# Performance work log

Hardware: AMD Instinct MI355X
Metric: run time of the kernel (lower is better)

Reference implementation:

```python
import jax, jax.numpy as jnp
import numpy as np
import math


def _strided_value_mask(L, S, dtype):
    # mask_line[L + d] == 0 when |d| is a power-of-two stride in {2,4,...,<=L};
    # value_mask[i, j] = mask_line[L - i + j], i.e. zero where |j - i| is such a stride.
    diff = jnp.abs(jnp.arange(L)[:, None] - jnp.arange(S)[None, :])  # [L, S]
    vm = jnp.ones((L, S), dtype=dtype)
    stride = 2
    while stride <= L:
        vm = vm * (diff != stride).astype(dtype)
        stride *= 2
    return vm


def setup_inputs() -> dict:
    key = jax.random.key(0)
    k1, k2, k3 = jax.random.split(key, 3)
    B, L, H, E = 4, 2048, 8, 64
    D = 64
    return {
        "queries": jax.random.normal(k1, (B, L, H, E), dtype=jnp.float32),
        "keys": jax.random.normal(k2, (B, L, H, E), dtype=jnp.float32),
        "values": jax.random.normal(k3, (B, L, H, D), dtype=jnp.float32),
    }


def reference(queries, keys, values):
    B, L, H, E = queries.shape
    S = keys.shape[1]
    scale = 1.0 / math.sqrt(E)

    # raw scores [B, H, L, S]
    scores = jnp.einsum("blhe,bshe->bhls", queries, keys)
    # multiplicative strided mask (zeroes scores at power-of-two offsets)
    vm = _strided_value_mask(L, S, scores.dtype)  # [L, S]
    scores = scores * vm
    # causal mask: upper triangle -> -inf (mask_flag=True, attn_mask=None path)
    causal = jnp.triu(jnp.ones((L, S), dtype=bool), k=1)
    scores = jnp.where(causal, -jnp.inf, scores)

    # dropout p=0.0 (eval) -> identity
    A = jax.nn.softmax(scale * scores, axis=-1)
    V = jnp.einsum("bhls,bshd->blhd", A, values)
    return V
```

## Files before the change

### kernel.cpp

```cpp
#include <hip/hip_runtime.h>
#include <hip/hip_bf16.h>
#include <stdint.h>

typedef __attribute__((ext_vector_type(8))) short short8;
typedef __attribute__((ext_vector_type(16))) float f32x16;

namespace {
constexpr int NB = 4, NL = 2048, NH = 8, NE = 64, ND = 64;
constexpr int KVBLK = 32;
constexpr float KS = 0.125f * 1.44269504f;
constexpr int NCHUNK = 40;
constexpr int RECSZ = 8320;
}

__device__ const unsigned char TG[NCHUNK] = {
  3,7,7,11,11,11,15,15,15,15, 10,10,14,14,14,14, 6,6,9,10, 13,13,13,13,
  9,9, 12,12,12,12, 2,5,5, 8,8,8, 4,4, 1, 0};
__device__ const unsigned char TT0[NCHUNK] = {
  0,0,16,0,16,32,0,16,32,48, 0,15,0,15,30,45, 0,14,0,30, 0,14,28,42,
  14,27, 0,13,26,39, 0,0,12, 0,12,24, 0,10, 0, 0};
__device__ const unsigned char TT1[NCHUNK] = {
  16,16,32,16,32,48,16,32,48,64, 15,30,15,30,45,60, 14,28,14,44, 14,28,42,56,
  27,40, 13,26,39,52, 12,12,24, 12,24,36, 10,20, 8, 4};
__device__ const unsigned char TREC[NCHUNK] = {
  3,10,11,21,22,23,36,37,38,39, 18,19,32,33,34,35, 8,9,15,20, 28,29,30,31,
  16,17, 24,25,26,27, 2,6,7, 12,13,14, 4,5, 1, 0};
__device__ const unsigned char CUMD[16] = {0,1,2,3,4,6,8,10,12,15,18,21,24,28,32,36};
__device__ const unsigned char NCHD[16] = {1,1,1,1,2,2,2,2,3,3,3,3,4,4,4,4};

__device__ __forceinline__ ushort bfb(float x) {
  __hip_bfloat16 b(x);
  return __builtin_bit_cast(ushort, b);
}
__device__ __forceinline__ uint32_t pkbf(float lo, float hi) {
  return (uint32_t)bfb(lo) | ((uint32_t)bfb(hi) << 16);
}

__global__ __launch_bounds__(256, 4)
void sattn_part(const float* __restrict__ Qg, const float* __restrict__ Kg,
                const float* __restrict__ Vg, float* __restrict__ W)
{
  const int id = blockIdx.x;
  const int bh = id & 31;
  const int e  = id >> 5;
  const int g  = TG[e];
  const int t0 = TT0[e], t1 = TT1[e];
  float* rec = W + (size_t)(bh * NCHUNK + TREC[e]) * RECSZ;
  const int b = bh >> 3, h = bh & 7;

  const int tid  = threadIdx.x;
  const int wave = tid >> 6;
  const int lane = tid & 63;
  const int ln31 = lane & 31;
  const int hi   = lane >> 5;

  __shared__ __align__(16) struct {
    ushort kt[KVBLK * 64];
    ushort vt[64 * 40];
  } lds;

  const int q0w = g * 128 + wave * 32;
  const int qi  = q0w + ln31;
  const int tw  = 4 * g + wave;

  short8 qf[4];
  {
    const float* qp = Qg + (((size_t)b * NL + qi) * NH + h) * NE;
    #pragma unroll
    for (int st = 0; st < 4; ++st) {
      const float* qpe = qp + st * 16 + hi * 8;
      union { short8 v; uint32_t u[4]; } f;
      #pragma unroll
      for (int j = 0; j < 4; ++j)
        f.u[j] = pkbf(qpe[2 * j] * KS, qpe[2 * j + 1] * KS);
      qf[st] = f.v;
    }
  }

  f32x16 acc0, acc1;
  #pragma unroll
  for (int i = 0; i < 16; ++i) { acc0[i] = 0.f; acc1[i] = 0.f; }
  float ls = 0.f;

  const int krow = tid >> 3,        kcol = (tid & 7) * 8;
  const int vrow = (tid >> 4) * 2,  vcol = (tid & 15) * 4;
  const float* kpp = Kg + (((size_t)b * NL + t0 * KVBLK + krow) * NH + h) * NE + kcol;
  const float* vpp = Vg + (((size_t)b * NL + t0 * KVBLK + vrow) * NH + h) * ND + vcol;
  constexpr int KSTEP = KVBLK * NH * NE;

  float kx[8], vx[8];
  #pragma unroll
  for (int j = 0; j < 8; ++j) kx[j] = kpp[j];
  #pragma unroll
  for (int j = 0; j < 4; ++j) { vx[j] = vpp[j]; vx[4 + j] = vpp[j + NH * ND]; }

  for (int t = t0; t < t1; ++t) {
    const int kv0 = t * KVBLK;
    __syncthreads();
    {
      uint32_t* kd = (uint32_t*)((char*)lds.kt + krow * 128 +
                                 ((kcol * 2) ^ ((krow & 7) << 4)));
      kd[0] = pkbf(kx[0], kx[1]); kd[1] = pkbf(kx[2], kx[3]);
      kd[2] = pkbf(kx[4], kx[5]); kd[3] = pkbf(kx[6], kx[7]);
      #pragma unroll
      for (int j = 0; j < 4; ++j) {
        int d = vcol + j;
        *(uint32_t*)((char*)lds.vt + d * 80 +
                     ((vrow * 2) ^ (((d >> 3) & 3) << 4))) = pkbf(vx[j], vx[4 + j]);
      }
    }
    {
      int tn = (t + 1 < t1) ? t + 1 : t;
      const float* kp = kpp + (size_t)(tn - t0) * KSTEP;
      const float* vp = vpp + (size_t)(tn - t0) * KSTEP;
      #pragma unroll
      for (int j = 0; j < 8; ++j) kx[j] = kp[j];
      #pragma unroll
      for (int j = 0; j < 4; ++j) { vx[j] = vp[j]; vx[4 + j] = vp[j + NH * ND]; }
    }
    __syncthreads();
    if (t > tw) continue;

    f32x16 s;
    #pragma unroll
    for (int i = 0; i < 16; ++i) s[i] = 0.f;
    const char* kb  = (const char*)lds.kt + ln31 * 128;
    const int   ksw = (ln31 & 7) << 4;
    __builtin_amdgcn_s_setprio(1);
    #pragma unroll
    for (int st = 0; st < 4; ++st) {
      short8 kf = *(const short8*)(kb + ((st * 32 + hi * 16) ^ ksw));
      s = __builtin_amdgcn_mfma_f32_32x32x16_bf16(kf, qf[st], s, 0, 0, 0);
    }
    __builtin_amdgcn_s_setprio(0);

    const int delta = q0w - kv0;
    const int qrelh = (qi - kv0) - 4 * hi;
    float ps0 = 0, ps1 = 0;
    if (t == tw) {
      #pragma unroll
      for (int r = 0; r < 16; ++r) {
        const int cr = (r & 3) + 8 * (r >> 2);
        int diff = qrelh - cr;
        float lg = s[r];
        bool p2 = (diff > 1) & ((diff & (diff - 1)) == 0);
        lg = p2 ? 0.f : lg;
        lg = (diff < 0) ? -__builtin_inff() : lg;
        float p = exp2f(lg);
        s[r] = p; (r & 1 ? ps1 : ps0) += p;
      }
    } else {
      int pmax = 1 << (31 - __clz(delta + 31));
      if (pmax >= delta - 31) {
        #pragma unroll
        for (int r = 0; r < 16; ++r) {
          const int cr = (r & 3) + 8 * (r >> 2);
          int diff = qrelh - cr;
          bool p2 = (diff > 1) & ((diff & (diff - 1)) == 0);
          float p = exp2f(p2 ? 0.f : s[r]);
          s[r] = p; (r & 1 ? ps1 : ps0) += p;
        }
      } else {
        #pragma unroll
        for (int r = 0; r < 16; ++r) {
          float p = exp2f(s[r]);
          s[r] = p; (r & 1 ? ps1 : ps0) += p;
        }
      }
    }
    ls += ps0 + ps1;

    uint32_t w0 = pkbf(s[0],  s[1]),  w1 = pkbf(s[2],  s[3]);
    uint32_t w2 = pkbf(s[4],  s[5]),  w3 = pkbf(s[6],  s[7]);
    uint32_t w4 = pkbf(s[8],  s[9]),  w5 = pkbf(s[10], s[11]);
    uint32_t w6 = pkbf(s[12], s[13]), w7 = pkbf(s[14], s[15]);
    uint32_t y0 = __shfl_xor(hi ? w0 : w2, 32);
    uint32_t y1 = __shfl_xor(hi ? w1 : w3, 32);
    uint32_t y2 = __shfl_xor(hi ? w4 : w6, 32);
    uint32_t y3 = __shfl_xor(hi ? w5 : w7, 32);
    union { short8 v; uint32_t u[4]; } f0, f1;
    if (hi == 0) {
      f0.u[0] = w0; f0.u[1] = w1; f0.u[2] = y0; f0.u[3] = y1;
      f1.u[0] = w4; f1.u[1] = w5; f1.u[2] = y2; f1.u[3] = y3;
    } else {
      f0.u[0] = y0; f0.u[1] = y1; f0.u[2] = w2; f0.u[3] = w3;
      f1.u[0] = y2; f1.u[1] = y3; f1.u[2] = w6; f1.u[3] = w7;
    }

    const char* vb = (const char*)lds.vt;
    const int d0 = ln31,      sw0 = ((d0 >> 3) & 3) << 4;
    const int d1 = 32 + ln31, sw1 = ((d1 >> 3) & 3) << 4;
    short8 a00 = *(const short8*)(vb + d0 * 80 + ((hi * 16) ^ sw0));
    short8 a01 = *(const short8*)(vb + d0 * 80 + ((32 + hi * 16) ^ sw0));
    short8 a10 = *(const short8*)(vb + d1 * 80 + ((hi * 16) ^ sw1));
    short8 a11 = *(const short8*)(vb + d1 * 80 + ((32 + hi * 16) ^ sw1));
    __builtin_amdgcn_s_setprio(1);
    acc0 = __builtin_amdgcn_mfma_f32_32x32x16_bf16(a00, f0.v, acc0, 0, 0, 0);
    acc0 = __builtin_amdgcn_mfma_f32_32x32x16_bf16(a01, f1.v, acc0, 0, 0, 0);
    acc1 = __builtin_amdgcn_mfma_f32_32x32x16_bf16(a10, f0.v, acc1, 0, 0, 0);
    acc1 = __builtin_amdgcn_mfma_f32_32x32x16_bf16(a11, f1.v, acc1, 0, 0, 0);
    __builtin_amdgcn_s_setprio(0);
  }

  ls += __shfl_xor(ls, 32);
  #pragma unroll
  for (int r = 0; r < 16; ++r) {
    int d = (r & 3) + 8 * (r >> 2) + 4 * hi;
    rec[d * 128 + wave * 32 + ln31]        = acc0[r];
    rec[(32 + d) * 128 + wave * 32 + ln31] = acc1[r];
  }
  if (hi == 0) rec[8192 + wave * 32 + ln31] = ls;
}

__global__ __launch_bounds__(256)
void sattn_combine(const float* __restrict__ W, float* __restrict__ Og)
{
  const int id = blockIdx.x;
  const int h2 = id & 1, g = (id >> 1) & 15, bh = id >> 5;
  const int b = bh >> 3, h = bh & 7;
  const int tid = threadIdx.x;

  __shared__ float sd[64][66];
  __shared__ float Lq[64];

  const float* rec0 = W + (size_t)(bh * NCHUNK + CUMD[g]) * RECSZ;
  const int nc = NCHD[g];

  #pragma unroll
  for (int rep = 0; rep < 16; ++rep) {
    int lin = rep * 256 + tid;
    int q = lin & 63, d = lin >> 6;
    float a = 0.f;
    for (int c = 0; c < nc; ++c) a += rec0[c * RECSZ + d * 128 + h2 * 64 + q];
    sd[d][q] = a;
  }
  if (tid < 64) {
    float a = 0.f;
    for (int c = 0; c < nc; ++c) a += rec0[c * RECSZ + 8192 + h2 * 64 + tid];
    Lq[tid] = 1.0f / a;
  }
  __syncthreads();
  #pragma unroll
  for (int rep = 0; rep < 16; ++rep) {
    int d = tid & 63, q = rep * 4 + (tid >> 6);
    float v = sd[d][q] * Lq[q];
    Og[(((size_t)b * NL + g * 128 + h2 * 64 + q) * NH + h) * ND + d] = v;
  }
}

__global__ __launch_bounds__(256)
void sattn_mono(const float* __restrict__ Qg, const float* __restrict__ Kg,
                const float* __restrict__ Vg, float* __restrict__ Og)
{
  const int bh = blockIdx.x;
  const int y  = blockIdx.y;
  const int qblk = (y < 8) ? (15 - y) : (y - 8);
  const int b = bh >> 3, h = bh & 7;
  const int tid  = threadIdx.x;
  const int wave = tid >> 6;
  const int lane = tid & 63;
  const int ln31 = lane & 31;
  const int hi   = lane >> 5;

  __shared__ __align__(16) union {
    struct { ushort kt[KVBLK * 64]; ushort vt[64 * 40]; } s;
    float ep[4 * 32 * 68];
  } lds;

  const int q0w = qblk * 128 + wave * 32;
  const int qi  = q0w + ln31;
  const int tw  = qblk * 4 + wave;
  const int NT  = qblk * 4 + 4;

  short8 qf[4];
  {
    const float* qp = Qg + (((size_t)b * NL + qi) * NH + h) * NE;
    #pragma unroll
    for (int st = 0; st < 4; ++st) {
      const float* qpe = qp + st * 16 + hi * 8;
      union { short8 v; uint32_t u[4]; } f;
      #pragma unroll
      for (int j = 0; j < 4; ++j) f.u[j] = pkbf(qpe[2 * j] * KS, qpe[2 * j + 1] * KS);
      qf[st] = f.v;
    }
  }
  f32x16 acc0, acc1;
  #pragma unroll
  for (int i = 0; i < 16; ++i) { acc0[i] = 0.f; acc1[i] = 0.f; }
  float ls = 0.f;

  const int krow = tid >> 3,        kcol = (tid & 7) * 8;
  const int vrow = (tid >> 4) * 2,  vcol = (tid & 15) * 4;
  const float* kpp = Kg + (((size_t)b * NL + krow) * NH + h) * NE + kcol;
  const float* vpp = Vg + (((size_t)b * NL + vrow) * NH + h) * ND + vcol;
  constexpr int KSTEP = KVBLK * NH * NE;

  float kx[8], vx[8];
  #pragma unroll
  for (int j = 0; j < 8; ++j) kx[j] = kpp[j];
  #pragma unroll
  for (int j = 0; j < 4; ++j) { vx[j] = vpp[j]; vx[4 + j] = vpp[j + NH * ND]; }

  for (int t = 0; t < NT; ++t) {
    const int kv0 = t * KVBLK;
    __syncthreads();
    {
      uint32_t* kd = (uint32_t*)((char*)lds.s.kt + krow * 128 +
                                 ((kcol * 2) ^ ((krow & 7) << 4)));
      kd[0] = pkbf(kx[0], kx[1]); kd[1] = pkbf(kx[2], kx[3]);
      kd[2] = pkbf(kx[4], kx[5]); kd[3] = pkbf(kx[6], kx[7]);
      #pragma unroll
      for (int j = 0; j < 4; ++j) {
        int d = vcol + j;
        *(uint32_t*)((char*)lds.s.vt + d * 80 +
                     ((vrow * 2) ^ (((d >> 3) & 3) << 4))) = pkbf(vx[j], vx[4 + j]);
      }
    }
    {
      int tn = (t + 1 < NT) ? t + 1 : t;
      const float* kp = kpp + (size_t)tn * KSTEP;
      const float* vp = vpp + (size_t)tn * KSTEP;
      #pragma unroll
      for (int j = 0; j < 8; ++j) kx[j] = kp[j];
      #pragma unroll
      for (int j = 0; j < 4; ++j) { vx[j] = vp[j]; vx[4 + j] = vp[j + NH * ND]; }
    }
    __syncthreads();
    if (t > tw) continue;

    f32x16 s;
    #pragma unroll
    for (int i = 0; i < 16; ++i) s[i] = 0.f;
    const char* kb  = (const char*)lds.s.kt + ln31 * 128;
    const int   ksw = (ln31 & 7) << 4;
    #pragma unroll
    for (int st = 0; st < 4; ++st) {
      short8 kf = *(const short8*)(kb + ((st * 32 + hi * 16) ^ ksw));
      s = __builtin_amdgcn_mfma_f32_32x32x16_bf16(kf, qf[st], s, 0, 0, 0);
    }
    const int delta = q0w - kv0;
    const int qrelh = (qi - kv0) - 4 * hi;
    float ps = 0.f;
    if (t == tw) {
      #pragma unroll
      for (int r = 0; r < 16; ++r) {
        const int cr = (r & 3) + 8 * (r >> 2);
        int diff = qrelh - cr;
        float lg = s[r];
        bool p2 = (diff > 1) & ((diff & (diff - 1)) == 0);
        lg = p2 ? 0.f : lg;
        lg = (diff < 0) ? -__builtin_inff() : lg;
        float p = exp2f(lg); s[r] = p; ps += p;
      }
    } else {
      int pmax = 1 << (31 - __clz(delta + 31));
      if (pmax >= delta - 31) {
        #pragma unroll
        for (int r = 0; r < 16; ++r) {
          const int cr = (r & 3) + 8 * (r >> 2);
          int diff = qrelh - cr;
          bool p2 = (diff > 1) & ((diff & (diff - 1)) == 0);
          float p = exp2f(p2 ? 0.f : s[r]); s[r] = p; ps += p;
        }
      } else {
        #pragma unroll
        for (int r = 0; r < 16; ++r) { float p = exp2f(s[r]); s[r] = p; ps += p; }
      }
    }
    ls += ps;

    uint32_t w0 = pkbf(s[0],  s[1]),  w1 = pkbf(s[2],  s[3]);
    uint32_t w2 = pkbf(s[4],  s[5]),  w3 = pkbf(s[6],  s[7]);
    uint32_t w4 = pkbf(s[8],  s[9]),  w5 = pkbf(s[10], s[11]);
    uint32_t w6 = pkbf(s[12], s[13]), w7 = pkbf(s[14], s[15]);
    uint32_t y0 = __shfl_xor(hi ? w0 : w2, 32);
    uint32_t y1 = __shfl_xor(hi ? w1 : w3, 32);
    uint32_t y2 = __shfl_xor(hi ? w4 : w6, 32);
    uint32_t y3 = __shfl_xor(hi ? w5 : w7, 32);
    union { short8 v; uint32_t u[4]; } f0, f1;
    if (hi == 0) {
      f0.u[0] = w0; f0.u[1] = w1; f0.u[2] = y0; f0.u[3] = y1;
      f1.u[0] = w4; f1.u[1] = w5; f1.u[2] = y2; f1.u[3] = y3;
    } else {
      f0.u[0] = y0; f0.u[1] = y1; f0.u[2] = w2; f0.u[3] = w3;
      f1.u[0] = y2; f1.u[1] = y3; f1.u[2] = w6; f1.u[3] = w7;
    }
    const char* vb = (const char*)lds.s.vt;
    const int d0 = ln31,      sw0 = ((d0 >> 3) & 3) << 4;
    const int d1 = 32 + ln31, sw1 = ((d1 >> 3) & 3) << 4;
    short8 a00 = *(const short8*)(vb + d0 * 80 + ((hi * 16) ^ sw0));
    short8 a01 = *(const short8*)(vb + d0 * 80 + ((32 + hi * 16) ^ sw0));
    short8 a10 = *(const short8*)(vb + d1 * 80 + ((hi * 16) ^ sw1));
    short8 a11 = *(const short8*)(vb + d1 * 80 + ((32 + hi * 16) ^ sw1));
    acc0 = __builtin_amdgcn_mfma_f32_32x32x16_bf16(a00, f0.v, acc0, 0, 0, 0);
    acc0 = __builtin_amdgcn_mfma_f32_32x32x16_bf16(a01, f1.v, acc0, 0, 0, 0);
    acc1 = __builtin_amdgcn_mfma_f32_32x32x16_bf16(a10, f0.v, acc1, 0, 0, 0);
    acc1 = __builtin_amdgcn_mfma_f32_32x32x16_bf16(a11, f1.v, acc1, 0, 0, 0);
  }

  __syncthreads();
  ls += __shfl_xor(ls, 32);
  const float inv = 1.0f / ls;
  float* ep = lds.ep + wave * (32 * 68);
  #pragma unroll
  for (int r = 0; r < 16; ++r) {
    int drow = (r & 3) + 8 * (r >> 2) + 4 * hi;
    ep[ln31 * 68 + drow]      = acc0[r] * inv;
    ep[ln31 * 68 + 32 + drow] = acc1[r] * inv;
  }
  __syncthreads();
  const float* epr = lds.ep + wave * (32 * 68);
  #pragma unroll
  for (int rep = 0; rep < 8; ++rep) {
    int q  = rep * 4 + (lane >> 4);
    int d4 = (lane & 15) * 4;
    float4 val = *(const float4*)(epr + q * 68 + d4);
    float* op = Og + (((size_t)b * NL + q0w + q) * NH + h) * ND + d4;
    *(float4*)op = val;
  }
}

extern "C" void kernel_launch(void* const* d_in, const int* in_sizes, int n_in,
                              void* d_out, int out_size, void* d_ws, size_t ws_size,
                              hipStream_t stream) {
  const float* Q = (const float*)d_in[0];
  const float* K = (const float*)d_in[1];
  const float* V = (const float*)d_in[2];
  float* O = (float*)d_out;
  const size_t need = (size_t)32 * NCHUNK * RECSZ * sizeof(float);
  if (ws_size >= need) {
    sattn_part<<<dim3(32 * NCHUNK), dim3(256), 0, stream>>>(Q, K, V, (float*)d_ws);
    sattn_combine<<<dim3(1024), dim3(256), 0, stream>>>((const float*)d_ws, O);
  } else {
    sattn_mono<<<dim3(32, 16), dim3(256), 0, stream>>>(Q, K, V, O);
  }
}
```

Baseline: 74.56 us.

## Double-buffer K/V tiles in LDS and vectorize combine kernel accesses

The partial-attention kernel now keeps two LDS buffers for K/V tiles and prefetches two tiles ahead. Each iteration stages the next tile while computing on the current one, so it needs only one barrier instead of two. Global loads become float4. The combine kernel reads partial records and writes output with float4, padding its LDS tile to 67 columns. This doubles LDS use per block and holds more prefetch registers, which could reduce occupancy.

```diff
diff --git a/kernel.cpp b/kernel.cpp
--- a/kernel.cpp
+++ b/kernel.cpp
@@ -11,6 +11,7 @@
 constexpr float KS = 0.125f * 1.44269504f;
 constexpr int NCHUNK = 40;
 constexpr int RECSZ = 8320;
+constexpr int BUFSZ = 9216;
 }
 
 __device__ const unsigned char TG[NCHUNK] = {
@@ -54,10 +55,9 @@
   const int ln31 = lane & 31;
   const int hi   = lane >> 5;
 
-  __shared__ __align__(16) struct {
-    ushort kt[KVBLK * 64];
-    ushort vt[64 * 40];
-  } lds;
+  __shared__ __align__(16) char smem[2 * BUFSZ];
+  char* B0 = smem;
+  char* B1 = smem + BUFSZ;
 
   const int q0w = g * 128 + wave * 32;
   const int qi  = q0w + ln31;
@@ -88,48 +88,36 @@
   const float* vpp = Vg + (((size_t)b * NL + t0 * KVBLK + vrow) * NH + h) * ND + vcol;
   constexpr int KSTEP = KVBLK * NH * NE;
 
-  float kx[8], vx[8];
-  #pragma unroll
-  for (int j = 0; j < 8; ++j) kx[j] = kpp[j];
-  #pragma unroll
-  for (int j = 0; j < 4; ++j) { vx[j] = vpp[j]; vx[4 + j] = vpp[j + NH * ND]; }
-
-  for (int t = t0; t < t1; ++t) {
+  auto LD = [&](int tn, float4& ka, float4& kb, float4& va, float4& vb) {
+    const float* kp = kpp + (size_t)(tn - t0) * KSTEP;
+    const float* vp = vpp + (size_t)(tn - t0) * KSTEP;
+    ka = *(const float4*)kp;  kb = *(const float4*)(kp + 4);
+    va = *(const float4*)vp;  vb = *(const float4*)(vp + NH * ND);
+  };
+  auto STG = [&](char* buf, const float4& ka, const float4& kb,
+                 const float4& va, const float4& vb) {
+    uint32_t* kd = (uint32_t*)(buf + krow * 128 + ((kcol * 2) ^ ((krow & 7) << 4)));
+    kd[0] = pkbf(ka.x, ka.y); kd[1] = pkbf(ka.z, ka.w);
+    kd[2] = pkbf(kb.x, kb.y); kd[3] = pkbf(kb.z, kb.w);
+    char* vb_ = buf + 4096;
+    const int sw = vrow * 2;
+    *(uint32_t*)(vb_ + (vcol+0)*80 + (sw ^ ((((vcol+0)>>3)&3)<<4))) = pkbf(va.x, vb.x);
+    *(uint32_t*)(vb_ + (vcol+1)*80 + (sw ^ ((((vcol+1)>>3)&3)<<4))) = pkbf(va.y, vb.y);
+    *(uint32_t*)(vb_ + (vcol+2)*80 + (sw ^ ((((vcol+2)>>3)&3)<<4))) = pkbf(va.z, vb.z);
+    *(uint32_t*)(vb_ + (vcol+3)*80 + (sw ^ ((((vcol+3)>>3)&3)<<4))) = pkbf(va.w, vb.w);
+  };
+
+  auto COMPUTE = [&](int t, const char* buf) {
     const int kv0 = t * KVBLK;
-    __syncthreads();
-    {
-      uint32_t* kd = (uint32_t*)((char*)lds.kt + krow * 128 +
-                                 ((kcol * 2) ^ ((krow & 7) << 4)));
-      kd[0] = pkbf(kx[0], kx[1]); kd[1] = pkbf(kx[2], kx[3]);
-      kd[2] = pkbf(kx[4], kx[5]); kd[3] = pkbf(kx[6], kx[7]);
-      #pragma unroll
-      for (int j = 0; j < 4; ++j) {
-        int d = vcol + j;
-        *(uint32_t*)((char*)lds.vt + d * 80 +
-                     ((vrow * 2) ^ (((d >> 3) & 3) << 4))) = pkbf(vx[j], vx[4 + j]);
-      }
-    }
-    {
-      int tn = (t + 1 < t1) ? t + 1 : t;
-      const float* kp = kpp + (size_t)(tn - t0) * KSTEP;
-      const float* vp = vpp + (size_t)(tn - t0) * KSTEP;
-      #pragma unroll
-      for (int j = 0; j < 8; ++j) kx[j] = kp[j];
-      #pragma unroll
-      for (int j = 0; j < 4; ++j) { vx[j] = vp[j]; vx[4 + j] = vp[j + NH * ND]; }
-    }
-    __syncthreads();
-    if (t > tw) continue;
-
     f32x16 s;
     #pragma unroll
     for (int i = 0; i < 16; ++i) s[i] = 0.f;
-    const char* kb  = (const char*)lds.kt + ln31 * 128;
+    const char* kb_ = buf + ln31 * 128;
     const int   ksw = (ln31 & 7) << 4;
     __builtin_amdgcn_s_setprio(1);
     #pragma unroll
     for (int st = 0; st < 4; ++st) {
-      short8 kf = *(const short8*)(kb + ((st * 32 + hi * 16) ^ ksw));
+      short8 kf = *(const short8*)(kb_ + ((st * 32 + hi * 16) ^ ksw));
       s = __builtin_amdgcn_mfma_f32_32x32x16_bf16(kf, qf[st], s, 0, 0, 0);
     }
     __builtin_amdgcn_s_setprio(0);
@@ -187,19 +175,41 @@
       f1.u[0] = y2; f1.u[1] = y3; f1.u[2] = w6; f1.u[3] = w7;
     }
 
-    const char* vb = (const char*)lds.vt;
+    const char* vb_ = buf + 4096;
     const int d0 = ln31,      sw0 = ((d0 >> 3) & 3) << 4;
     const int d1 = 32 + ln31, sw1 = ((d1 >> 3) & 3) << 4;
-    short8 a00 = *(const short8*)(vb + d0 * 80 + ((hi * 16) ^ sw0));
-    short8 a01 = *(const short8*)(vb + d0 * 80 + ((32 + hi * 16) ^ sw0));
-    short8 a10 = *(const short8*)(vb + d1 * 80 + ((hi * 16) ^ sw1));
-    short8 a11 = *(const short8*)(vb + d1 * 80 + ((32 + hi * 16) ^ sw1));
+    short8 a00 = *(const short8*)(vb_ + d0 * 80 + ((hi * 16) ^ sw0));
+    short8 a01 = *(const short8*)(vb_ + d0 * 80 + ((32 + hi * 16) ^ sw0));
+    short8 a10 = *(const short8*)(vb_ + d1 * 80 + ((hi * 16) ^ sw1));
+    short8 a11 = *(const short8*)(vb_ + d1 * 80 + ((32 + hi * 16) ^ sw1));
     __builtin_amdgcn_s_setprio(1);
     acc0 = __builtin_amdgcn_mfma_f32_32x32x16_bf16(a00, f0.v, acc0, 0, 0, 0);
     acc0 = __builtin_amdgcn_mfma_f32_32x32x16_bf16(a01, f1.v, acc0, 0, 0, 0);
     acc1 = __builtin_amdgcn_mfma_f32_32x32x16_bf16(a10, f0.v, acc1, 0, 0, 0);
     acc1 = __builtin_amdgcn_mfma_f32_32x32x16_bf16(a11, f1.v, acc1, 0, 0, 0);
     __builtin_amdgcn_s_setprio(0);
+  };
+
+  float4 ka0, kb0, va0, vb0, ka1, kb1, va1, vb1;
+  LD(t0, ka0, kb0, va0, vb0);
+  STG(B0, ka0, kb0, va0, vb0);
+  LD(t0 + 1, ka1, kb1, va1, vb1);
+  __syncthreads();
+
+  int t = t0;
+  while (true) {
+    int tn = (t + 2 < t1) ? t + 2 : t1 - 1;
+    LD(tn, ka0, kb0, va0, vb0);
+    STG(B1, ka1, kb1, va1, vb1);
+    if (t <= tw) COMPUTE(t, B0);
+    __syncthreads();
+    if (++t >= t1) break;
+    tn = (t + 2 < t1) ? t + 2 : t1 - 1;
+    LD(tn, ka1, kb1, va1, vb1);
+    STG(B0, ka0, kb0, va0, vb0);
+    if (t <= tw) COMPUTE(t, B1);
+    __syncthreads();
+    if (++t >= t1) break;
   }
 
   ls += __shfl_xor(ls, 32);
@@ -220,31 +230,37 @@
   const int b = bh >> 3, h = bh & 7;
   const int tid = threadIdx.x;
 
-  __shared__ float sd[64][66];
+  __shared__ float sd[64][67];
   __shared__ float Lq[64];
 
   const float* rec0 = W + (size_t)(bh * NCHUNK + CUMD[g]) * RECSZ;
   const int nc = NCHD[g];
 
   #pragma unroll
-  for (int rep = 0; rep < 16; ++rep) {
-    int lin = rep * 256 + tid;
-    int q = lin & 63, d = lin >> 6;
-    float a = 0.f;
-    for (int c = 0; c < nc; ++c) a += rec0[c * RECSZ + d * 128 + h2 * 64 + q];
-    sd[d][q] = a;
+  for (int rep = 0; rep < 4; ++rep) {
+    int d  = rep * 16 + (tid >> 4);
+    int q4 = (tid & 15) * 4;
+    float4 a = {0.f, 0.f, 0.f, 0.f};
+    for (int c = 0; c < nc; ++c) {
+      float4 v = *(const float4*)(rec0 + (size_t)c * RECSZ + d * 128 + h2 * 64 + q4);
+      a.x += v.x; a.y += v.y; a.z += v.z; a.w += v.w;
+    }
+    sd[d][q4 + 0] = a.x; sd[d][q4 + 1] = a.y;
+    sd[d][q4 + 2] = a.z; sd[d][q4 + 3] = a.w;
   }
   if (tid < 64) {
     float a = 0.f;
-    for (int c = 0; c < nc; ++c) a += rec0[c * RECSZ + 8192 + h2 * 64 + tid];
+    for (int c = 0; c < nc; ++c) a += rec0[(size_t)c * RECSZ + 8192 + h2 * 64 + tid];
     Lq[tid] = 1.0f / a;
   }
   __syncthreads();
   #pragma unroll
-  for (int rep = 0; rep < 16; ++rep) {
-    int d = tid & 63, q = rep * 4 + (tid >> 6);
-    float v = sd[d][q] * Lq[q];
-    Og[(((size_t)b * NL + g * 128 + h2 * 64 + q) * NH + h) * ND + d] = v;
+  for (int rep = 0; rep < 4; ++rep) {
+    int q  = rep * 16 + (tid >> 4);
+    int d4 = (tid & 15) * 4;
+    float l = Lq[q];
+    float4 o = { sd[d4][q] * l, sd[d4 + 1][q] * l, sd[d4 + 2][q] * l, sd[d4 + 3][q] * l };
+    *(float4*)(Og + (((size_t)b * NL + g * 128 + h2 * 64 + q) * NH + h) * ND + d4) = o;
   }
 }
 
```

New measurement: 93.11 us. 24.9% more time.
